# Kernel optimization log

Measured on AMD Instinct MI355X. Metric: run time of the kernel, lower is better.

Reference implementation:

```python
import jax, jax.numpy as jnp
import numpy as np

TOP_K = 2
NORM_TOPK = True


def setup_inputs() -> dict:
    key = jax.random.key(0)
    k1, k2, k3, k4 = jax.random.split(key, 4)
    B, S, H = 2, 1024, 2048
    E, I = 16, 768
    hidden_states = jax.random.normal(k1, (B, S, H), dtype=jnp.float32)
    gate_w = jax.random.normal(k2, (E, H), dtype=jnp.float32) * 0.02
    gate_up_w = jax.random.normal(k3, (E, 2 * I, H), dtype=jnp.float32) * 0.02
    down_w = jax.random.normal(k4, (E, H, I), dtype=jnp.float32) * 0.02
    return {
        "hidden_states": hidden_states,
        "gate_w": gate_w,
        "gate_up_w": gate_up_w,
        "down_w": down_w,
        "top_k": TOP_K,
    }


def reference(hidden_states, gate_w, gate_up_w, down_w, top_k):
    B, S, H = hidden_states.shape
    E = gate_w.shape[0]
    x = hidden_states.reshape(-1, H)  # [T, H]
    T = x.shape[0]

    # Router: softmax in float32 (as in torch F.softmax(..., dtype=torch.float))
    router_logits = x @ gate_w.T  # [T, E]
    probs = jax.nn.softmax(router_logits.astype(jnp.float32), axis=-1)
    top_w, top_idx = jax.lax.top_k(probs, top_k)  # [T, k]
    if NORM_TOPK:
        top_w = top_w / jnp.sum(top_w, axis=-1, keepdims=True)
    top_w = top_w.astype(x.dtype)

    # Dense combine weights [T, E]: routing weight where selected, 0 elsewhere.
    comb = jnp.sum(jax.nn.one_hot(top_idx, E, dtype=x.dtype) * top_w[..., None], axis=1)

    # SwiGLU expert MLPs evaluated for all experts, combined with sparse weights.
    gu = jnp.einsum("th,efh->tef", x, gate_up_w)  # [T, E, 2I]
    g, u = jnp.split(gu, 2, axis=-1)
    h = jax.nn.silu(g) * u  # [T, E, I]
    y = jnp.einsum("tei,ehi->teh", h, down_w)  # [T, E, H]
    out = jnp.einsum("teh,te->th", y, comb)  # [T, H]

    return out.reshape(B, S, H), router_logits
```

## Files before the change

### kernel.cpp

```cpp
#include <hip/hip_runtime.h>
#include <hip/hip_bf16.h>
#include <stdint.h>

#define T_TOK 2048
#define H_DIM 2048
#define E_NUM 16
#define I_DIM 768

typedef __bf16 bf16;
typedef __bf16 bf16x4 __attribute__((ext_vector_type(4)));
typedef __bf16 bf16x8 __attribute__((ext_vector_type(8)));
typedef float f32x4 __attribute__((ext_vector_type(4)));

__device__ __forceinline__ void async_cp16(void* l, const void* g) {
    __builtin_amdgcn_global_load_lds(
        (const __attribute__((address_space(1))) void*)g,
        (__attribute__((address_space(3))) void*)l, 16, 0, 0);
}

__global__ __launch_bounds__(256) void router_kernel(
    const float* __restrict__ x, const float* __restrict__ gw,
    float* __restrict__ logits, int* __restrict__ cnt,
    int* __restrict__ tok_list, float* __restrict__ wgt_list,
    bf16* __restrict__ xb)
{
    const int t = blockIdx.x;
    const int tid = threadIdx.x;
    const int lane = tid & 63, wid = tid >> 6;

    double part[E_NUM];
#pragma unroll
    for (int e = 0; e < E_NUM; ++e) part[e] = 0.0;

#pragma unroll
    for (int it = 0; it < 2; ++it) {
        int h = it * 1024 + tid * 4;
        float4 xv = *(const float4*)(x + (size_t)t * H_DIM + h);
        bf16x4 xb4 = { (bf16)xv.x, (bf16)xv.y, (bf16)xv.z, (bf16)xv.w };
        *(bf16x4*)(xb + (size_t)t * H_DIM + h) = xb4;
#pragma unroll
        for (int e = 0; e < E_NUM; ++e) {
            float4 wv = *(const float4*)(gw + (size_t)e * H_DIM + h);
            part[e] += (double)xv.x * (double)wv.x + (double)xv.y * (double)wv.y
                     + (double)xv.z * (double)wv.z + (double)xv.w * (double)wv.w;
        }
    }
#pragma unroll
    for (int off = 32; off > 0; off >>= 1)
#pragma unroll
        for (int e = 0; e < E_NUM; ++e)
            part[e] += __shfl_down(part[e], off);

    __shared__ double sh[4][E_NUM];
    __shared__ float lg[E_NUM];
    if (lane == 0)
#pragma unroll
        for (int e = 0; e < E_NUM; ++e) sh[wid][e] = part[e];
    __syncthreads();
    if (tid < E_NUM) {
        float v = (float)(sh[0][tid] + sh[1][tid] + sh[2][tid] + sh[3][tid]);
        lg[tid] = v;
        logits[(size_t)t * E_NUM + tid] = v;
    }
    __syncthreads();
    if (tid == 0) {
        int i0 = 0; float v0 = lg[0];
#pragma unroll
        for (int e = 1; e < E_NUM; ++e) if (lg[e] > v0) { v0 = lg[e]; i0 = e; }
        int i1 = -1; float v1 = -3.4e38f;
#pragma unroll
        for (int e = 0; e < E_NUM; ++e) if (e != i0 && lg[e] > v1) { v1 = lg[e]; i1 = e; }
        float w0 = 1.0f / (1.0f + __expf(v1 - v0));
        float w1 = 1.0f - w0;
        int p0 = atomicAdd(&cnt[i0], 1);
        tok_list[i0 * T_TOK + p0] = t; wgt_list[i0 * T_TOK + p0] = w0;
        int p1 = atomicAdd(&cnt[i1], 1);
        tok_list[i1 * T_TOK + p1] = t; wgt_list[i1 * T_TOK + p1] = w1;
    }
}

__global__ void scan_kernel(const int* __restrict__ cnt, int* __restrict__ offs)
{
    if (threadIdx.x == 0) {
        int o = 0;
        for (int e = 0; e < E_NUM; ++e) { offs[e] = o; o += cnt[e]; }
    }
}

__global__ __launch_bounds__(256, 4) void gateup_kernel(
    const bf16* __restrict__ xb, const float* __restrict__ gup,
    const int* __restrict__ cnt, const int* __restrict__ offs,
    const int* __restrict__ tok_list, bf16* __restrict__ hbuf)
{
    const int e = blockIdx.z;
    const int count = cnt[e];
    const int row0 = blockIdx.y * 64;
    if (row0 >= count) return;
    const int i0 = blockIdx.x * 64;
    const int hoff = offs[e];
    const int tid = threadIdx.x;
    const int lane = tid & 63, wid = tid >> 6;

    __shared__ __align__(16) bf16 As[64 * 64];
    __shared__ __align__(16) float Bs[128 * 64];

    int raA0 = tid >> 3, sA0 = tid & 7;
    int raA1 = raA0 + 32;
    int cA0 = sA0 ^ (raA0 & 7);
    int cA1 = sA0 ^ (raA1 & 7);
    int tr0 = row0 + raA0; if (tr0 >= count) tr0 = count - 1;
    int tr1 = row0 + raA1; if (tr1 >= count) tr1 = count - 1;
    const bf16* srcA0 = xb + (size_t)tok_list[e * T_TOK + tr0] * H_DIM + cA0 * 8;
    const bf16* srcA1 = xb + (size_t)tok_list[e * T_TOK + tr1] * H_DIM + cA1 * 8;
    bf16* dstA0 = As + (size_t)(wid * 64) * 8;
    bf16* dstA1 = As + (size_t)(wid * 64 + 256) * 8;

    const float* srcB[8]; float* dstB[8];
#pragma unroll
    for (int i = 0; i < 8; ++i) {
        int idx = i * 256 + tid;
        int r = idx >> 4, s = idx & 15;
        int c = s ^ (r & 15);
        int is_u = (r >> 5) & 1;
        int ioff = (r >> 6) * 32 + (r & 31);
        size_t grow = (size_t)e * (2 * I_DIM) + (size_t)is_u * I_DIM + i0 + ioff;
        srcB[i] = gup + grow * H_DIM + c * 4;
        dstB[i] = Bs + (size_t)(i * 256 + wid * 64) * 4;
    }

    f32x4 acc[2][4];
#pragma unroll
    for (int a = 0; a < 2; ++a)
#pragma unroll
        for (int b = 0; b < 4; ++b) acc[a][b] = (f32x4){0.f, 0.f, 0.f, 0.f};

    const int la = lane & 15, lq = lane >> 4;
    const int wm = wid >> 1, wn = wid & 1;

    for (int k0 = 0; k0 < H_DIM; k0 += 64) {
        async_cp16(dstA0, srcA0 + k0);
        async_cp16(dstA1, srcA1 + k0);
#pragma unroll
        for (int i = 0; i < 8; ++i) async_cp16(dstB[i], srcB[i] + k0);
        __syncthreads();
#pragma unroll
        for (int ks = 0; ks < 2; ++ks) {
            bf16x8 af[2], bfr[4];
            int chA = ks * 4 + lq;
            int c0 = ks * 8 + lq * 2;
#pragma unroll
            for (int mt = 0; mt < 2; ++mt) {
                int row = 32 * wm + 16 * mt + la;
                int sl = chA ^ (row & 7);
                af[mt] = *(const bf16x8*)(As + (size_t)(row * 8 + sl) * 8);
            }
#pragma unroll
            for (int nt = 0; nt < 4; ++nt) {
                int row = 64 * wn + 16 * nt + la;
                int s0 = c0 ^ (row & 15);
                int s1 = s0 ^ 1;
                f32x4 v0 = *(const f32x4*)(Bs + (size_t)(row * 16 + s0) * 4);
                f32x4 v1 = *(const f32x4*)(Bs + (size_t)(row * 16 + s1) * 4);
                bfr[nt] = (bf16x8){ (bf16)v0.x, (bf16)v0.y, (bf16)v0.z, (bf16)v0.w,
                                    (bf16)v1.x, (bf16)v1.y, (bf16)v1.z, (bf16)v1.w };
            }
#pragma unroll
            for (int mt = 0; mt < 2; ++mt)
#pragma unroll
                for (int nt = 0; nt < 4; ++nt)
                    acc[mt][nt] = __builtin_amdgcn_mfma_f32_16x16x32_bf16(af[mt], bfr[nt], acc[mt][nt], 0, 0, 0);
        }
        __syncthreads();
    }

#pragma unroll
    for (int mt = 0; mt < 2; ++mt)
#pragma unroll
        for (int p = 0; p < 2; ++p)
#pragma unroll
            for (int r = 0; r < 4; ++r) {
                int trow = 32 * wm + 16 * mt + lq * 4 + r;
                if (row0 + trow < count) {
                    float g = acc[mt][p][r], u = acc[mt][p + 2][r];
                    float hv = (g / (1.0f + __expf(-g))) * u;
                    int col = i0 + 32 * wn + 16 * p + la;
                    hbuf[(size_t)(hoff + row0 + trow) * I_DIM + col] = (bf16)hv;
                }
            }
}

__global__ __launch_bounds__(256, 4) void down_kernel(
    const float* __restrict__ dw, const bf16* __restrict__ hbuf,
    const int* __restrict__ cnt, const int* __restrict__ offs,
    const int* __restrict__ tok_list, const float* __restrict__ wgt_list,
    float* __restrict__ out)
{
    const int e = blockIdx.z;
    const int count = cnt[e];
    const int row0 = blockIdx.y * 64;
    if (row0 >= count) return;
    const int n0 = blockIdx.x * 128;
    const int hoff = offs[e];
    const int tid = threadIdx.x;
    const int lane = tid & 63, wid = tid >> 6;

    __shared__ __align__(16) bf16 As[64 * 64];
    __shared__ __align__(16) float Bs[128 * 64];

    int raA0 = tid >> 3, sA0 = tid & 7;
    int raA1 = raA0 + 32;
    int cA0 = sA0 ^ (raA0 & 7);
    int cA1 = sA0 ^ (raA1 & 7);
    int ar0 = row0 + raA0; if (ar0 >= count) ar0 = count - 1;
    int ar1 = row0 + raA1; if (ar1 >= count) ar1 = count - 1;
    const bf16* srcA0 = hbuf + (size_t)(hoff + ar0) * I_DIM + cA0 * 8;
    const bf16* srcA1 = hbuf + (size_t)(hoff + ar1) * I_DIM + cA1 * 8;
    bf16* dstA0 = As + (size_t)(wid * 64) * 8;
    bf16* dstA1 = As + (size_t)(wid * 64 + 256) * 8;

    const float* srcB[8]; float* dstB[8];
#pragma unroll
    for (int i = 0; i < 8; ++i) {
        int idx = i * 256 + tid;
        int r = idx >> 4, s = idx & 15;
        int c = s ^ (r & 15);
        srcB[i] = dw + ((size_t)e * H_DIM + n0 + r) * I_DIM + c * 4;
        dstB[i] = Bs + (size_t)(i * 256 + wid * 64) * 4;
    }

    f32x4 acc[2][4];
#pragma unroll
    for (int a = 0; a < 2; ++a)
#pragma unroll
        for (int b = 0; b < 4; ++b) acc[a][b] = (f32x4){0.f, 0.f, 0.f, 0.f};

    const int la = lane & 15, lq = lane >> 4;
    const int wm = wid >> 1, wn = wid & 1;

    for (int k0 = 0; k0 < I_DIM; k0 += 64) {
        async_cp16(dstA0, srcA0 + k0);
        async_cp16(dstA1, srcA1 + k0);
#pragma unroll
        for (int i = 0; i < 8; ++i) async_cp16(dstB[i], srcB[i] + k0);
        __syncthreads();
#pragma unroll
        for (int ks = 0; ks < 2; ++ks) {
            bf16x8 af[2], bfr[4];
            int chA = ks * 4 + lq;
            int c0 = ks * 8 + lq * 2;
#pragma unroll
            for (int mt = 0; mt < 2; ++mt) {
                int row = 32 * wm + 16 * mt + la;
                int sl = chA ^ (row & 7);
                af[mt] = *(const bf16x8*)(As + (size_t)(row * 8 + sl) * 8);
            }
#pragma unroll
            for (int nt = 0; nt < 4; ++nt) {
                int row = 64 * wn + 16 * nt + la;
                int s0 = c0 ^ (row & 15);
                int s1 = s0 ^ 1;
                f32x4 v0 = *(const f32x4*)(Bs + (size_t)(row * 16 + s0) * 4);
                f32x4 v1 = *(const f32x4*)(Bs + (size_t)(row * 16 + s1) * 4);
                bfr[nt] = (bf16x8){ (bf16)v0.x, (bf16)v0.y, (bf16)v0.z, (bf16)v0.w,
                                    (bf16)v1.x, (bf16)v1.y, (bf16)v1.z, (bf16)v1.w };
            }
#pragma unroll
            for (int mt = 0; mt < 2; ++mt)
#pragma unroll
                for (int nt = 0; nt < 4; ++nt)
                    acc[mt][nt] = __builtin_amdgcn_mfma_f32_16x16x32_bf16(af[mt], bfr[nt], acc[mt][nt], 0, 0, 0);
        }
        __syncthreads();
    }

#pragma unroll
    for (int mt = 0; mt < 2; ++mt)
#pragma unroll
        for (int nt = 0; nt < 4; ++nt)
#pragma unroll
            for (int r = 0; r < 4; ++r) {
                int trow = 32 * wm + 16 * mt + lq * 4 + r;
                if (row0 + trow < count) {
                    int col = n0 + 64 * wn + 16 * nt + la;
                    int grow = row0 + trow;
                    atomicAdd(&out[(size_t)tok_list[e * T_TOK + grow] * H_DIM + col],
                              wgt_list[e * T_TOK + grow] * acc[mt][nt][r]);
                }
            }
}

extern "C" void kernel_launch(void* const* d_in, const int* in_sizes, int n_in,
                              void* d_out, int out_size, void* d_ws, size_t ws_size,
                              hipStream_t stream)
{
    const float* x   = (const float*)d_in[0];
    const float* gw  = (const float*)d_in[1];
    const float* gup = (const float*)d_in[2];
    const float* dw  = (const float*)d_in[3];
    float* out = (float*)d_out;
    float* logits = out + (size_t)T_TOK * H_DIM;

    char* ws = (char*)d_ws;
    int*   cnt      = (int*)(ws + 0);
    int*   offs     = (int*)(ws + 256);
    int*   tok_list = (int*)(ws + 512);
    float* wgt_list = (float*)(ws + 131584);
    bf16*  hbuf     = (bf16*)(ws + 262656);
    bf16*  xb       = (bf16*)(ws + 6554112);

    hipMemsetAsync(cnt, 0, 256, stream);
    hipMemsetAsync(out, 0, (size_t)T_TOK * H_DIM * sizeof(float), stream);

    router_kernel<<<T_TOK, 256, 0, stream>>>(x, gw, logits, cnt, tok_list, wgt_list, xb);
    scan_kernel<<<1, 64, 0, stream>>>(cnt, offs);
    gateup_kernel<<<dim3(I_DIM / 64, T_TOK / 64, E_NUM), 256, 0, stream>>>(
        xb, gup, cnt, offs, tok_list, hbuf);
    down_kernel<<<dim3(H_DIM / 128, T_TOK / 64, E_NUM), 256, 0, stream>>>(
        dw, hbuf, cnt, offs, tok_list, wgt_list, out);
}
```

Baseline: 529.8 us.

## Enlarge MoE GEMM token tiles to 128 rows and reorder grid for weight reuse

Both expert GEMM kernels now process 128 token rows per block instead of 64. Each wave owns 32 rows across the full 128-wide N tile with 2x8 MFMA accumulators, and the grid is reordered so the token-tile index is fastest. This halves how often the fp32 weights are re-read from global memory and converted per token, at the cost of more registers and LDS per block (launch bounds drop to 3 blocks per CU) and more wasted work on partial tiles. The router reduction also switches from wave shuffles to a two-stage LDS reduction using a large shared buffer.

Result: slower. 995.2 us (+87.9%).

```diff
diff --git a/kernel.cpp b/kernel.cpp
--- a/kernel.cpp
+++ b/kernel.cpp
@@ -26,7 +26,6 @@
 {
     const int t = blockIdx.x;
     const int tid = threadIdx.x;
-    const int lane = tid & 63, wid = tid >> 6;
 
     double part[E_NUM];
 #pragma unroll
@@ -45,20 +44,26 @@
                      + (double)xv.z * (double)wv.z + (double)xv.w * (double)wv.w;
         }
     }
-#pragma unroll
-    for (int off = 32; off > 0; off >>= 1)
-#pragma unroll
-        for (int e = 0; e < E_NUM; ++e)
-            part[e] += __shfl_down(part[e], off);
-
-    __shared__ double sh[4][E_NUM];
+
+    __shared__ double red[E_NUM][256];
+    __shared__ double red2[E_NUM][16];
     __shared__ float lg[E_NUM];
-    if (lane == 0)
-#pragma unroll
-        for (int e = 0; e < E_NUM; ++e) sh[wid][e] = part[e];
+#pragma unroll
+    for (int e = 0; e < E_NUM; ++e) red[e][tid] = part[e];
+    __syncthreads();
+    {
+        int e = tid >> 4, seg = tid & 15;
+        double s = 0.0;
+#pragma unroll
+        for (int j = 0; j < 16; ++j) s += red[e][seg * 16 + j];
+        red2[e][seg] = s;
+    }
     __syncthreads();
     if (tid < E_NUM) {
-        float v = (float)(sh[0][tid] + sh[1][tid] + sh[2][tid] + sh[3][tid]);
+        double s = 0.0;
+#pragma unroll
+        for (int j = 0; j < 16; ++j) s += red2[tid][j];
+        float v = (float)s;
         lg[tid] = v;
         logits[(size_t)t * E_NUM + tid] = v;
     }
@@ -87,87 +92,82 @@
     }
 }
 
-__global__ __launch_bounds__(256, 4) void gateup_kernel(
+__global__ __launch_bounds__(256, 3) void gateup_kernel(
     const bf16* __restrict__ xb, const float* __restrict__ gup,
     const int* __restrict__ cnt, const int* __restrict__ offs,
     const int* __restrict__ tok_list, bf16* __restrict__ hbuf)
 {
     const int e = blockIdx.z;
     const int count = cnt[e];
-    const int row0 = blockIdx.y * 64;
+    const int row0 = blockIdx.x * 128;
     if (row0 >= count) return;
-    const int i0 = blockIdx.x * 64;
+    const int i0 = blockIdx.y * 64;
     const int hoff = offs[e];
     const int tid = threadIdx.x;
     const int lane = tid & 63, wid = tid >> 6;
 
-    __shared__ __align__(16) bf16 As[64 * 64];
+    __shared__ __align__(16) bf16 As[128 * 64];
     __shared__ __align__(16) float Bs[128 * 64];
 
-    int raA0 = tid >> 3, sA0 = tid & 7;
-    int raA1 = raA0 + 32;
-    int cA0 = sA0 ^ (raA0 & 7);
-    int cA1 = sA0 ^ (raA1 & 7);
-    int tr0 = row0 + raA0; if (tr0 >= count) tr0 = count - 1;
-    int tr1 = row0 + raA1; if (tr1 >= count) tr1 = count - 1;
-    const bf16* srcA0 = xb + (size_t)tok_list[e * T_TOK + tr0] * H_DIM + cA0 * 8;
-    const bf16* srcA1 = xb + (size_t)tok_list[e * T_TOK + tr1] * H_DIM + cA1 * 8;
-    bf16* dstA0 = As + (size_t)(wid * 64) * 8;
-    bf16* dstA1 = As + (size_t)(wid * 64 + 256) * 8;
-
+    const bf16* srcA[4]; bf16* dstA[4];
+#pragma unroll
+    for (int i = 0; i < 4; ++i) {
+        int idx = i * 256 + tid;
+        int r = idx >> 3, s = idx & 7;
+        int c = s ^ (r & 7);
+        int tr = row0 + r; if (tr >= count) tr = count - 1;
+        srcA[i] = xb + (size_t)tok_list[e * T_TOK + tr] * H_DIM + c * 8;
+        dstA[i] = As + (size_t)(i * 256 + wid * 64) * 8;
+    }
     const float* srcB[8]; float* dstB[8];
 #pragma unroll
     for (int i = 0; i < 8; ++i) {
         int idx = i * 256 + tid;
         int r = idx >> 4, s = idx & 15;
         int c = s ^ (r & 15);
-        int is_u = (r >> 5) & 1;
-        int ioff = (r >> 6) * 32 + (r & 31);
-        size_t grow = (size_t)e * (2 * I_DIM) + (size_t)is_u * I_DIM + i0 + ioff;
+        size_t grow = (size_t)e * (2 * I_DIM) + ((r >> 6) ? I_DIM : 0) + i0 + (r & 63);
         srcB[i] = gup + grow * H_DIM + c * 4;
         dstB[i] = Bs + (size_t)(i * 256 + wid * 64) * 4;
     }
 
-    f32x4 acc[2][4];
+    f32x4 acc[2][8];
 #pragma unroll
     for (int a = 0; a < 2; ++a)
 #pragma unroll
-        for (int b = 0; b < 4; ++b) acc[a][b] = (f32x4){0.f, 0.f, 0.f, 0.f};
+        for (int b = 0; b < 8; ++b) acc[a][b] = (f32x4){0.f, 0.f, 0.f, 0.f};
 
     const int la = lane & 15, lq = lane >> 4;
-    const int wm = wid >> 1, wn = wid & 1;
 
     for (int k0 = 0; k0 < H_DIM; k0 += 64) {
-        async_cp16(dstA0, srcA0 + k0);
-        async_cp16(dstA1, srcA1 + k0);
+#pragma unroll
+        for (int i = 0; i < 4; ++i) async_cp16(dstA[i], srcA[i] + k0);
 #pragma unroll
         for (int i = 0; i < 8; ++i) async_cp16(dstB[i], srcB[i] + k0);
         __syncthreads();
 #pragma unroll
         for (int ks = 0; ks < 2; ++ks) {
-            bf16x8 af[2], bfr[4];
             int chA = ks * 4 + lq;
             int c0 = ks * 8 + lq * 2;
+            bf16x8 af[2], bfr[8];
 #pragma unroll
             for (int mt = 0; mt < 2; ++mt) {
-                int row = 32 * wm + 16 * mt + la;
+                int row = 32 * wid + 16 * mt + la;
                 int sl = chA ^ (row & 7);
                 af[mt] = *(const bf16x8*)(As + (size_t)(row * 8 + sl) * 8);
             }
 #pragma unroll
-            for (int nt = 0; nt < 4; ++nt) {
-                int row = 64 * wn + 16 * nt + la;
+            for (int nt = 0; nt < 8; ++nt) {
+                int row = 16 * nt + la;
                 int s0 = c0 ^ (row & 15);
-                int s1 = s0 ^ 1;
                 f32x4 v0 = *(const f32x4*)(Bs + (size_t)(row * 16 + s0) * 4);
-                f32x4 v1 = *(const f32x4*)(Bs + (size_t)(row * 16 + s1) * 4);
+                f32x4 v1 = *(const f32x4*)(Bs + (size_t)(row * 16 + (s0 ^ 1)) * 4);
                 bfr[nt] = (bf16x8){ (bf16)v0.x, (bf16)v0.y, (bf16)v0.z, (bf16)v0.w,
                                     (bf16)v1.x, (bf16)v1.y, (bf16)v1.z, (bf16)v1.w };
             }
 #pragma unroll
             for (int mt = 0; mt < 2; ++mt)
 #pragma unroll
-                for (int nt = 0; nt < 4; ++nt)
+                for (int nt = 0; nt < 8; ++nt)
                     acc[mt][nt] = __builtin_amdgcn_mfma_f32_16x16x32_bf16(af[mt], bfr[nt], acc[mt][nt], 0, 0, 0);
         }
         __syncthreads();
@@ -176,20 +176,20 @@
 #pragma unroll
     for (int mt = 0; mt < 2; ++mt)
 #pragma unroll
-        for (int p = 0; p < 2; ++p)
+        for (int nt = 0; nt < 4; ++nt)
 #pragma unroll
             for (int r = 0; r < 4; ++r) {
-                int trow = 32 * wm + 16 * mt + lq * 4 + r;
+                int trow = 32 * wid + 16 * mt + lq * 4 + r;
                 if (row0 + trow < count) {
-                    float g = acc[mt][p][r], u = acc[mt][p + 2][r];
+                    float g = acc[mt][nt][r], u = acc[mt][nt + 4][r];
                     float hv = (g / (1.0f + __expf(-g))) * u;
-                    int col = i0 + 32 * wn + 16 * p + la;
+                    int col = i0 + 16 * nt + la;
                     hbuf[(size_t)(hoff + row0 + trow) * I_DIM + col] = (bf16)hv;
                 }
             }
 }
 
-__global__ __launch_bounds__(256, 4) void down_kernel(
+__global__ __launch_bounds__(256, 3) void down_kernel(
     const float* __restrict__ dw, const bf16* __restrict__ hbuf,
     const int* __restrict__ cnt, const int* __restrict__ offs,
     const int* __restrict__ tok_list, const float* __restrict__ wgt_list,
@@ -197,27 +197,26 @@
 {
     const int e = blockIdx.z;
     const int count = cnt[e];
-    const int row0 = blockIdx.y * 64;
+    const int row0 = blockIdx.x * 128;
     if (row0 >= count) return;
-    const int n0 = blockIdx.x * 128;
+    const int n0 = blockIdx.y * 128;
     const int hoff = offs[e];
     const int tid = threadIdx.x;
     const int lane = tid & 63, wid = tid >> 6;
 
-    __shared__ __align__(16) bf16 As[64 * 64];
+    __shared__ __align__(16) bf16 As[128 * 64];
     __shared__ __align__(16) float Bs[128 * 64];
 
-    int raA0 = tid >> 3, sA0 = tid & 7;
-    int raA1 = raA0 + 32;
-    int cA0 = sA0 ^ (raA0 & 7);
-    int cA1 = sA0 ^ (raA1 & 7);
-    int ar0 = row0 + raA0; if (ar0 >= count) ar0 = count - 1;
-    int ar1 = row0 + raA1; if (ar1 >= count) ar1 = count - 1;
-    const bf16* srcA0 = hbuf + (size_t)(hoff + ar0) * I_DIM + cA0 * 8;
-    const bf16* srcA1 = hbuf + (size_t)(hoff + ar1) * I_DIM + cA1 * 8;
-    bf16* dstA0 = As + (size_t)(wid * 64) * 8;
-    bf16* dstA1 = As + (size_t)(wid * 64 + 256) * 8;
-
+    const bf16* srcA[4]; bf16* dstA[4];
+#pragma unroll
+    for (int i = 0; i < 4; ++i) {
+        int idx = i * 256 + tid;
+        int r = idx >> 3, s = idx & 7;
+        int c = s ^ (r & 7);
+        int tr = row0 + r; if (tr >= count) tr = count - 1;
+        srcA[i] = hbuf + (size_t)(hoff + tr) * I_DIM + c * 8;
+        dstA[i] = As + (size_t)(i * 256 + wid * 64) * 8;
+    }
     const float* srcB[8]; float* dstB[8];
 #pragma unroll
     for (int i = 0; i < 8; ++i) {
@@ -228,46 +227,44 @@
         dstB[i] = Bs + (size_t)(i * 256 + wid * 64) * 4;
     }
 
-    f32x4 acc[2][4];
+    f32x4 acc[2][8];
 #pragma unroll
     for (int a = 0; a < 2; ++a)
 #pragma unroll
-        for (int b = 0; b < 4; ++b) acc[a][b] = (f32x4){0.f, 0.f, 0.f, 0.f};
+        for (int b = 0; b < 8; ++b) acc[a][b] = (f32x4){0.f, 0.f, 0.f, 0.f};
 
     const int la = lane & 15, lq = lane >> 4;
-    const int wm = wid >> 1, wn = wid & 1;
 
     for (int k0 = 0; k0 < I_DIM; k0 += 64) {
-        async_cp16(dstA0, srcA0 + k0);
-        async_cp16(dstA1, srcA1 + k0);
+#pragma unroll
+        for (int i = 0; i < 4; ++i) async_cp16(dstA[i], srcA[i] + k0);
 #pragma unroll
         for (int i = 0; i < 8; ++i) async_cp16(dstB[i], srcB[i] + k0);
         __syncthreads();
 #pragma unroll
         for (int ks = 0; ks < 2; ++ks) {
-            bf16x8 af[2], bfr[4];
             int chA = ks * 4 + lq;
             int c0 = ks * 8 + lq * 2;
+            bf16x8 af[2], bfr[8];
 #pragma unroll
             for (int mt = 0; mt < 2; ++mt) {
-                int row = 32 * wm + 16 * mt + la;
+                int row = 32 * wid + 16 * mt + la;
                 int sl = chA ^ (row & 7);
                 af[mt] = *(const bf16x8*)(As + (size_t)(row * 8 + sl) * 8);
             }
 #pragma unroll
-            for (int nt = 0; nt < 4; ++nt) {
-                int row = 64 * wn + 16 * nt + la;
+            for (int nt = 0; nt < 8; ++nt) {
+                int row = 16 * nt + la;
                 int s0 = c0 ^ (row & 15);
-                int s1 = s0 ^ 1;
                 f32x4 v0 = *(const f32x4*)(Bs + (size_t)(row * 16 + s0) * 4);
-                f32x4 v1 = *(const f32x4*)(Bs + (size_t)(row * 16 + s1) * 4);
+                f32x4 v1 = *(const f32x4*)(Bs + (size_t)(row * 16 + (s0 ^ 1)) * 4);
                 bfr[nt] = (bf16x8){ (bf16)v0.x, (bf16)v0.y, (bf16)v0.z, (bf16)v0.w,
                                     (bf16)v1.x, (bf16)v1.y, (bf16)v1.z, (bf16)v1.w };
             }
 #pragma unroll
             for (int mt = 0; mt < 2; ++mt)
 #pragma unroll
-                for (int nt = 0; nt < 4; ++nt)
+                for (int nt = 0; nt < 8; ++nt)
                     acc[mt][nt] = __builtin_amdgcn_mfma_f32_16x16x32_bf16(af[mt], bfr[nt], acc[mt][nt], 0, 0, 0);
         }
         __syncthreads();
@@ -276,12 +273,12 @@
 #pragma unroll
     for (int mt = 0; mt < 2; ++mt)
 #pragma unroll
-        for (int nt = 0; nt < 4; ++nt)
+        for (int nt = 0; nt < 8; ++nt)
 #pragma unroll
             for (int r = 0; r < 4; ++r) {
-                int trow = 32 * wm + 16 * mt + lq * 4 + r;
+                int trow = 32 * wid + 16 * mt + lq * 4 + r;
                 if (row0 + trow < count) {
-                    int col = n0 + 64 * wn + 16 * nt + la;
+                    int col = n0 + 16 * nt + la;
                     int grow = row0 + trow;
                     atomicAdd(&out[(size_t)tok_list[e * T_TOK + grow] * H_DIM + col],
                               wgt_list[e * T_TOK + grow] * acc[mt][nt][r]);
@@ -313,8 +310,8 @@
 
     router_kernel<<<T_TOK, 256, 0, stream>>>(x, gw, logits, cnt, tok_list, wgt_list, xb);
     scan_kernel<<<1, 64, 0, stream>>>(cnt, offs);
-    gateup_kernel<<<dim3(I_DIM / 64, T_TOK / 64, E_NUM), 256, 0, stream>>>(
+    gateup_kernel<<<dim3(T_TOK / 128, I_DIM / 64, E_NUM), 256, 0, stream>>>(
         xb, gup, cnt, offs, tok_list, hbuf);
-    down_kernel<<<dim3(H_DIM / 128, T_TOK / 64, E_NUM), 256, 0, stream>>>(
+    down_kernel<<<dim3(T_TOK / 128, H_DIM / 128, E_NUM), 256, 0, stream>>>(
         dw, hbuf, cnt, offs, tok_list, wgt_list, out);
 }
```
